# Performance work log

Measured on AMD Instinct MI355X. Metric: run time of the kernel, lower is better.

## Reference

```python
import jax, jax.numpy as jnp
import numpy as np

N_NODES = 10000
NEG_SLOPE = 0.2  # PyG GATv2Conv default


def gatv2(x, src, dst, Wl, bl, Wr, br, att, bias, n_nodes):
    """Single-head GATv2Conv (PyG defaults: heads=1, concat=True, self-loops added by caller)."""
    xl = x @ Wl + bl            # [N, dout] message source transform (lin_l)
    xr = x @ Wr + br            # [N, dout] target transform (lin_r)
    h = jax.nn.leaky_relu(xl[src] + xr[dst], NEG_SLOPE)   # [E, dout]
    e = h @ att                                            # [E] attention logits
    m = jax.ops.segment_max(e, dst, num_segments=n_nodes)  # per-target max
    ex = jnp.exp(e - m[dst])
    s = jax.ops.segment_sum(ex, dst, num_segments=n_nodes)
    alpha = ex / s[dst]                                    # segment softmax over incoming edges
    out = jax.ops.segment_sum(alpha[:, None] * xl[src], dst, num_segments=n_nodes)
    return out + bias


def _glorot(key, shape, scale=0.05):
    return jax.random.normal(key, shape, dtype=jnp.float32) * scale


def setup_inputs() -> dict:
    key = jax.random.key(0)
    ks = jax.random.split(key, 20)
    d_in, d0, d1 = 1000, 256, 128
    E = 320000
    x = jax.random.normal(ks[0], (N_NODES, d_in), dtype=jnp.float32)
    edge_index = jax.random.randint(ks[1], (2, E), 0, N_NODES, dtype=jnp.int64)
    return {
        "x": x,
        "edge_index": edge_index,
        # proj_in: d_in -> 256
        "Wpi": _glorot(ks[2], (d_in, d0)), "bpi": jnp.zeros((d0,), jnp.float32),
        # enc GATv2Conv 256 -> 128
        "Wl1": _glorot(ks[3], (d0, d1)), "bl1": jnp.zeros((d1,), jnp.float32),
        "Wr1": _glorot(ks[4], (d0, d1)), "br1": jnp.zeros((d1,), jnp.float32),
        "att1": _glorot(ks[5], (d1,)), "bias1": jnp.zeros((d1,), jnp.float32),
        # dec GATv2Conv 128 -> 256
        "Wl2": _glorot(ks[6], (d1, d0)), "bl2": jnp.zeros((d0,), jnp.float32),
        "Wr2": _glorot(ks[7], (d1, d0)), "br2": jnp.zeros((d0,), jnp.float32),
        "att2": _glorot(ks[8], (d0,)), "bias2": jnp.zeros((d0,), jnp.float32),
        # proj_out: 256 -> d_in
        "Wpo": _glorot(ks[9], (d0, d_in)), "bpo": jnp.zeros((d_in,), jnp.float32),
    }


def reference(x, edge_index, Wpi, bpi, Wl1, bl1, Wr1, br1, att1, bias1,
              Wl2, bl2, Wr2, br2, att2, bias2, Wpo, bpo):
    n = x.shape[0]
    # add self-loops (PyG GATv2Conv default add_self_loops=True)
    loops = jnp.arange(n, dtype=edge_index.dtype)
    src = jnp.concatenate([edge_index[0], loops])
    dst = jnp.concatenate([edge_index[1], loops])
    h = x @ Wpi + bpi
    z = gatv2(h, src, dst, Wl1, bl1, Wr1, br1, att1, bias1, n)
    d = gatv2(z, src, dst, Wl2, bl2, Wr2, br2, att2, bias2, n)
    x_hat = d @ Wpo + bpo
    return (x_hat, z)
```

## Files before the change

kernel.cpp:

```cpp
#include <hip/hip_runtime.h>
#include <math.h>

#define N_NODES 10000
#define MPAD    10112
#define D_IN    1000
#define KPAD_IN 1024
#define D0      256
#define D1      128
#define NPAD_OUT 1024
#define NEG_SLOPE 0.2f

typedef __attribute__((ext_vector_type(8))) short short8;
typedef __attribute__((ext_vector_type(4))) float f32x4;

__device__ __forceinline__ ushort f2bf(float f) {
  union { float f; unsigned u; } c; c.f = f;
  unsigned r = c.u + 0x7FFF + ((c.u >> 16) & 1);
  return (ushort)(r >> 16);
}
__device__ __forceinline__ float bf2f(ushort b) {
  union { unsigned u; float f; } c; c.u = ((unsigned)b) << 16;
  return c.f;
}


__global__ void count_kernel(const int* __restrict__ idx, int E, int n, int* __restrict__ counts) {
  int k = blockIdx.x * blockDim.x + threadIdx.x;
  int tot = E + n;
  if (k >= tot) return;
  int dst = (k < E) ? idx[E + k] : (k - E);
  atomicAdd(&counts[dst], 1);
}

__global__ void scan_kernel(const int* __restrict__ counts, int* __restrict__ offsets,
                            int* __restrict__ cursors, int n) {
  __shared__ int tsum[1024];
  int tid = threadIdx.x;
  int per = (n + 1023) / 1024;
  int start = tid * per;
  int end = start + per; if (end > n) end = n;
  int s = 0;
  for (int i = start; i < end; i++) s += counts[i];
  tsum[tid] = s;
  __syncthreads();
  for (int off = 1; off < 1024; off <<= 1) {
    int v = (tid >= off) ? tsum[tid - off] : 0;
    __syncthreads();
    if (tid >= off) tsum[tid] += v;
    __syncthreads();
  }
  int run = (tid == 0) ? 0 : tsum[tid - 1];
  for (int i = start; i < end; i++) {
    offsets[i] = run; cursors[i] = run;
    run += counts[i];
  }
  if (tid == 1023) offsets[n] = tsum[1023];
}

__global__ void scatter_kernel(const int* __restrict__ idx, int E, int n,
                               int* __restrict__ cursors, int* __restrict__ srcs) {
  int k = blockIdx.x * blockDim.x + threadIdx.x;
  int tot = E + n;
  if (k >= tot) return;
  int src, dst;
  if (k < E) { src = idx[k]; dst = idx[E + k]; }
  else       { src = k - E;  dst = src; }
  int pos = atomicAdd(&cursors[dst], 1);
  srcs[pos] = src;
}


#define T_WPI   (256 * 1024)
#define T_W1    (256 * 256)
#define T_W2    (512 * 128)
#define T_WPO   (1024 * 256)
#define OFF_W1  T_WPI
#define OFF_W2  (OFF_W1 + T_W1)
#define OFF_WPO (OFF_W2 + T_W2)
#define OFF_B   (OFF_WPO + T_WPO)
#define T_ALL   (OFF_B + 768)
#define CONV_T  (MPAD * 256)
#define PREP_T  (CONV_T + T_ALL + N_NODES)

__global__ void prep_all(const float* __restrict__ x, ushort* __restrict__ xb,
                         const float* __restrict__ Wpi,
                         const float* __restrict__ Wl1, const float* __restrict__ Wr1,
                         const float* __restrict__ Wl2, const float* __restrict__ Wr2,
                         const float* __restrict__ Wpo,
                         const float* __restrict__ bl1, const float* __restrict__ br1,
                         const float* __restrict__ bl2, const float* __restrict__ br2,
                         ushort* __restrict__ Wpi_t, ushort* __restrict__ W1cat,
                         ushort* __restrict__ W2cat, ushort* __restrict__ Wpo_t,
                         float* __restrict__ bcat1, float* __restrict__ bcat2,
                         int* __restrict__ counts) {
  int idx = blockIdx.x * 256 + threadIdx.x;
  if (idx < CONV_T) {
    int r = idx >> 8, k4 = (idx & 255) * 4;
    ushort4 o = {0, 0, 0, 0};
    if (r < N_NODES && k4 < D_IN) {
      float4 v = *(const float4*)(x + (size_t)r * D_IN + k4);
      o.x = f2bf(v.x); o.y = f2bf(v.y); o.z = f2bf(v.z); o.w = f2bf(v.w);
    }
    *(ushort4*)(xb + (size_t)idx * 4) = o;
    return;
  }
  int j = idx - CONV_T;
  if (j < OFF_W1) {
    int n = j >> 10, k = j & 1023;
    Wpi_t[j] = f2bf((k < 1000) ? Wpi[(size_t)k * 256 + n] : 0.f);
  } else if (j < OFF_W2) {
    int q = j - OFF_W1, n = q >> 8, k = q & 255;
    float v = (n < 128) ? Wl1[k * 128 + n] : Wr1[k * 128 + (n - 128)];
    W1cat[q] = f2bf(v);
  } else if (j < OFF_WPO) {
    int q = j - OFF_W2, n = q >> 7, k = q & 127;
    float v = (n < 256) ? Wl2[k * 256 + n] : Wr2[k * 256 + (n - 256)];
    W2cat[q] = f2bf(v);
  } else if (j < OFF_B) {
    int q = j - OFF_WPO, n = q >> 8, k = q & 255;
    Wpo_t[q] = f2bf((n < 1000) ? Wpo[(size_t)k * 1000 + n] : 0.f);
  } else if (j < T_ALL) {
    int q = j - OFF_B;
    if (q < 128)      bcat1[q] = bl1[q];
    else if (q < 256) bcat1[q] = br1[q - 128];
    else if (q < 512) bcat2[q - 256] = bl2[q - 256];
    else              bcat2[q - 256] = br2[q - 512];
  } else {
    int q = j - T_ALL;
    if (q < N_NODES) counts[q] = 0;
  }
}


template<int MODE>
__launch_bounds__(256)
__global__ void gemm_mfma(const ushort* __restrict__ A, int lda,
                          const ushort* __restrict__ Bt, int ldb,
                          const float* __restrict__ bias,
                          float* __restrict__ Cf, ushort* __restrict__ Cb, int ldp,
                          int M_valid, int N_valid, int K) {
  constexpr int BK = 32;
  __shared__ ushort As[64 * BK];
  __shared__ ushort Bs[64 * BK];
  const int tid  = threadIdx.x;
  const int lane = tid & 63, wave = tid >> 6;
  const int wr = wave >> 1, wc = wave & 1;
  const int bm = blockIdx.y * 64, bn = blockIdx.x * 64;
  const int r16 = lane & 15, kb = lane >> 4;

  f32x4 acc[2][2] = {};

  const int srow = tid >> 2;
  const int scol = (tid & 3) * 8;
  const ushort* Ag = A  + (size_t)(bm + srow) * lda + scol;
  const ushort* Bg = Bt + (size_t)(bn + srow) * ldb + scol;

  for (int k0 = 0; k0 < K; k0 += BK) {
    __builtin_amdgcn_global_load_lds((const __attribute__((address_space(1))) void*)(Ag + k0),
                                     (__attribute__((address_space(3))) void*)(As + tid * 8), 16, 0, 0);
    __builtin_amdgcn_global_load_lds((const __attribute__((address_space(1))) void*)(Bg + k0),
                                     (__attribute__((address_space(3))) void*)(Bs + tid * 8), 16, 0, 0);
    __syncthreads();

    short8 af[2], bfr[2];
    #pragma unroll
    for (int mi = 0; mi < 2; mi++)
      af[mi] = *(const short8*)(As + ((wr * 32 + mi * 16 + r16) * BK + kb * 8));
    #pragma unroll
    for (int ni = 0; ni < 2; ni++)
      bfr[ni] = *(const short8*)(Bs + ((wc * 32 + ni * 16 + r16) * BK + kb * 8));
    #pragma unroll
    for (int mi = 0; mi < 2; mi++)
      #pragma unroll
      for (int ni = 0; ni < 2; ni++)
        acc[mi][ni] = __builtin_amdgcn_mfma_f32_16x16x32_bf16(af[mi], bfr[ni], acc[mi][ni], 0, 0, 0);
    __syncthreads();
  }

  #pragma unroll
  for (int mi = 0; mi < 2; mi++) {
    const int row = bm + wr * 32 + mi * 16 + (lane >> 4) * 4;
    #pragma unroll
    for (int ni = 0; ni < 2; ni++) {
      const int col = bn + wc * 32 + ni * 16 + r16;
      const float bv = (col < N_valid) ? bias[col] : 0.f;
      #pragma unroll
      for (int r = 0; r < 4; r++) {
        const int gr = row + r;
        const float val = acc[mi][ni][r] + bv;
        if constexpr (MODE == 0) {
          if (gr < M_valid && col < N_valid) Cf[(size_t)gr * ldp + col] = val;
        } else if constexpr (MODE == 1) {
          Cb[(size_t)gr * ldp + col] = f2bf(gr < M_valid ? val : 0.f);
        } else {
          if (col < ldp) Cb[(size_t)gr * ldp + col] = f2bf(val);
          else           Cf[(size_t)gr * ldp + (col - ldp)] = val;
        }
      }
    }
  }
}


template<int D>
__launch_bounds__(256)
__global__ void gat_fused(const ushort* __restrict__ xlb, const float* __restrict__ xrf,
                          const float* __restrict__ att, const float* __restrict__ bias,
                          const int* __restrict__ offsets, const int* __restrict__ srcs,
                          float* __restrict__ out_f32, ushort* __restrict__ out_bf16,
                          int n_valid) {
  constexpr int EPL = D / 64;
  const int v    = blockIdx.x;
  const int tid  = threadIdx.x;
  const int lane = tid & 63;
  const int wave = tid >> 6;
  const int d0   = lane * EPL;

  if (v >= n_valid) {
    if (out_bf16 && tid < D) out_bf16[(size_t)v * D + tid] = 0;
    return;
  }

  __shared__ float m_s[4];
  __shared__ float s_s[4];
  __shared__ float buf[4][D];

  float rv[EPL], av[EPL], acc[EPL];
  #pragma unroll
  for (int d = 0; d < EPL; d++) {
    rv[d]  = xrf[(size_t)v * D + d0 + d];
    av[d]  = att[d0 + d];
    acc[d] = 0.f;
  }

  const int beg = offsets[v], end = offsets[v + 1];
  float m = -INFINITY, s = 0.f;

  int k = beg + wave;
  ushort xnxt[EPL];
  if (k < end) {
    const int u0 = srcs[k];
    if constexpr (EPL == 4) *(ushort4*)xnxt = *(const ushort4*)(xlb + (size_t)u0 * D + d0);
    else                    *(ushort2*)xnxt = *(const ushort2*)(xlb + (size_t)u0 * D + d0);
  }

  for (; k < end; k += 4) {
    ushort xcur[EPL];
    #pragma unroll
    for (int d = 0; d < EPL; d++) xcur[d] = xnxt[d];

    const int kn = k + 4;
    if (kn < end) {
      const int un = srcs[kn];
      if constexpr (EPL == 4) *(ushort4*)xnxt = *(const ushort4*)(xlb + (size_t)un * D + d0);
      else                    *(ushort2*)xnxt = *(const ushort2*)(xlb + (size_t)un * D + d0);
    }

    float xv[EPL], p = 0.f;
    #pragma unroll
    for (int d = 0; d < EPL; d++) {
      xv[d] = bf2f(xcur[d]);
      float t = xv[d] + rv[d];
      t = fmaxf(t, NEG_SLOPE * t);
      p = fmaf(t, av[d], p);
    }
    #pragma unroll
    for (int off = 32; off > 0; off >>= 1) p += __shfl_xor(p, off);

    if (p <= m + 8.f) {
      const float w = __expf(p - m);
      s += w;
      #pragma unroll
      for (int d = 0; d < EPL; d++) acc[d] = fmaf(w, xv[d], acc[d]);
    } else {
      const float cold = __expf(m - p);
      s = fmaf(s, cold, 1.f);
      #pragma unroll
      for (int d = 0; d < EPL; d++) acc[d] = fmaf(acc[d], cold, xv[d]);
      m = p;
    }
  }

  if (lane == 0) m_s[wave] = m;
  __syncthreads();
  const float M = fmaxf(fmaxf(m_s[0], m_s[1]), fmaxf(m_s[2], m_s[3]));
  const float c = __expf(m - M);
  if (lane == 0) s_s[wave] = s * c;
  #pragma unroll
  for (int d = 0; d < EPL; d++) buf[wave][d0 + d] = acc[d] * c;
  __syncthreads();

  if (tid < D) {
    const float stot = s_s[0] + s_s[1] + s_s[2] + s_s[3];
    const float val = (buf[0][tid] + buf[1][tid] + buf[2][tid] + buf[3][tid]) / stot + bias[tid];
    if (out_f32)  out_f32[(size_t)v * D + tid] = val;
    if (out_bf16) out_bf16[(size_t)v * D + tid] = f2bf(val);
  }
}


extern "C" void kernel_launch(void* const* d_in, const int* in_sizes, int n_in,
                              void* d_out, int out_size, void* d_ws, size_t ws_size,
                              hipStream_t stream) {
  const float* x     = (const float*)d_in[0];
  const int*   eidx  = (const int*)d_in[1];
  const float* Wpi   = (const float*)d_in[2];
  const float* bpi   = (const float*)d_in[3];
  const float* Wl1   = (const float*)d_in[4];
  const float* bl1   = (const float*)d_in[5];
  const float* Wr1   = (const float*)d_in[6];
  const float* br1   = (const float*)d_in[7];
  const float* att1  = (const float*)d_in[8];
  const float* bias1 = (const float*)d_in[9];
  const float* Wl2   = (const float*)d_in[10];
  const float* bl2   = (const float*)d_in[11];
  const float* Wr2   = (const float*)d_in[12];
  const float* br2   = (const float*)d_in[13];
  const float* att2  = (const float*)d_in[14];
  const float* bias2 = (const float*)d_in[15];
  const float* Wpo   = (const float*)d_in[16];
  const float* bpo   = (const float*)d_in[17];

  const int E    = in_sizes[1] / 2;
  const int n    = N_NODES;
  const int Etot = E + n;

  float* out_xhat = (float*)d_out;
  float* out_z    = (float*)d_out + (size_t)N_NODES * D_IN;

  char* wp = (char*)d_ws;
  auto alloc = [&](size_t bytes) { char* p = wp; wp += (bytes + 255) & ~(size_t)255; return p; };
  char* regionA = (char*)alloc((size_t)MPAD * KPAD_IN * 2);
  ushort* hb_db = (ushort*)alloc((size_t)MPAD * D0 * 2);
  ushort* zb    = (ushort*)alloc((size_t)MPAD * D1 * 2);
  int* counts  = (int*)alloc((size_t)n * 4);
  int* offsets = (int*)alloc((size_t)(n + 1) * 4);
  int* cursors = (int*)alloc((size_t)n * 4);
  int* srcs    = (int*)alloc((size_t)Etot * 4);
  ushort* Wpi_t = (ushort*)alloc((size_t)T_WPI * 2);
  ushort* W1cat = (ushort*)alloc((size_t)T_W1 * 2);
  ushort* W2cat = (ushort*)alloc((size_t)T_W2 * 2);
  ushort* Wpo_t = (ushort*)alloc((size_t)T_WPO * 2);
  float*  bcat1 = (float*)alloc(256 * 4);
  float*  bcat2 = (float*)alloc(512 * 4);

  ushort* xb   = (ushort*)regionA;
  float*  xr1f = (float*)regionA;
  ushort* xl1b = (ushort*)(regionA + 8 * 1024 * 1024);
  float*  xr2f = (float*)regionA;
  ushort* xl2b = (ushort*)(regionA + 12 * 1024 * 1024);
  ushort* hb   = hb_db;
  ushort* db   = hb_db;

  prep_all<<<(PREP_T + 255) / 256, 256, 0, stream>>>(
      x, xb, Wpi, Wl1, Wr1, Wl2, Wr2, Wpo, bl1, br1, bl2, br2,
      Wpi_t, W1cat, W2cat, Wpo_t, bcat1, bcat2, counts);
  const int tb = 256;
  count_kernel<<<(Etot + tb - 1) / tb, tb, 0, stream>>>(eidx, E, n, counts);
  scan_kernel<<<1, 1024, 0, stream>>>(counts, offsets, cursors, n);
  scatter_kernel<<<(Etot + tb - 1) / tb, tb, 0, stream>>>(eidx, E, n, cursors, srcs);

  gemm_mfma<1><<<dim3(D0 / 64, MPAD / 64), 256, 0, stream>>>(
      xb, KPAD_IN, Wpi_t, KPAD_IN, bpi, nullptr, hb, D0, N_NODES, D0, KPAD_IN);
  gemm_mfma<2><<<dim3(256 / 64, MPAD / 64), 256, 0, stream>>>(
      hb, D0, W1cat, D0, bcat1, xr1f, xl1b, D1, N_NODES, 256, D0);
  gat_fused<D1><<<MPAD, 256, 0, stream>>>(xl1b, xr1f, att1, bias1,
                                          offsets, srcs, out_z, zb, N_NODES);
  gemm_mfma<2><<<dim3(512 / 64, MPAD / 64), 256, 0, stream>>>(
      zb, D1, W2cat, D1, bcat2, xr2f, xl2b, D0, N_NODES, 512, D1);
  gat_fused<D0><<<MPAD, 256, 0, stream>>>(xl2b, xr2f, att2, bias2,
                                          offsets, srcs, nullptr, db, N_NODES);
  gemm_mfma<0><<<dim3(NPAD_OUT / 64, MPAD / 64), 256, 0, stream>>>(
      db, D0, Wpo_t, D0, bpo, out_xhat, nullptr, D_IN, N_NODES, D_IN, D0);
}
```

Before: 322.3 us.

## Process multiple edges per wave using sub-wave lane groups in GAT aggregation

Each wave in the fused GATv2 kernel is split into groups of D/16 lanes. Each lane handles 16 features through two 16-byte bf16 loads, so a block now processes 16 edges (D=256) or 32 edges (D=128) per step instead of 4. This cuts the shuffle reduction depth, widens memory accesses and raises edge-level parallelism. The data-dependent branch in the online softmax is replaced by branchless predicated updates. The cost is more registers and shared memory, a longer cross-group combine at the end, and wasted lanes at the tail for low-degree nodes.

Result: faster. 307.4 us (-4.6%).

```diff
diff --git a/kernel.cpp b/kernel.cpp
--- a/kernel.cpp
+++ b/kernel.cpp
@@ -209,90 +209,108 @@
                           const int* __restrict__ offsets, const int* __restrict__ srcs,
                           float* __restrict__ out_f32, ushort* __restrict__ out_bf16,
                           int n_valid) {
-  constexpr int EPL = D / 64;
+  constexpr int G    = D / 16;
+  constexpr int LOGG = (D == 256) ? 4 : 3;
+  constexpr int NGW  = 64 / G;
+  constexpr int NG   = 4 * NGW;
+  constexpr int H    = D / 2;
+
   const int v    = blockIdx.x;
   const int tid  = threadIdx.x;
   const int lane = tid & 63;
   const int wave = tid >> 6;
-  const int d0   = lane * EPL;
+  const int sub  = lane & (G - 1);
+  const int grp  = wave * NGW + (lane >> LOGG);
+  const int d0   = sub * 8;
 
   if (v >= n_valid) {
     if (out_bf16 && tid < D) out_bf16[(size_t)v * D + tid] = 0;
     return;
   }
 
-  __shared__ float m_s[4];
-  __shared__ float s_s[4];
-  __shared__ float buf[4][D];
-
-  float rv[EPL], av[EPL], acc[EPL];
+  __shared__ float m_s[NG];
+  __shared__ float s_s[NG];
+  __shared__ float buf[NG][D];
+
+  float rv[16], av[16], acc[16];
   #pragma unroll
-  for (int d = 0; d < EPL; d++) {
-    rv[d]  = xrf[(size_t)v * D + d0 + d];
-    av[d]  = att[d0 + d];
-    acc[d] = 0.f;
+  for (int i = 0; i < 8; i++) {
+    rv[i]     = xrf[(size_t)v * D + d0 + i];
+    rv[8 + i] = xrf[(size_t)v * D + H + d0 + i];
+    av[i]     = att[d0 + i];
+    av[8 + i] = att[H + d0 + i];
+    acc[i] = 0.f; acc[8 + i] = 0.f;
   }
 
   const int beg = offsets[v], end = offsets[v + 1];
-  float m = -INFINITY, s = 0.f;
-
-  int k = beg + wave;
-  ushort xnxt[EPL];
-  if (k < end) {
-    const int u0 = srcs[k];
-    if constexpr (EPL == 4) *(ushort4*)xnxt = *(const ushort4*)(xlb + (size_t)u0 * D + d0);
-    else                    *(ushort2*)xnxt = *(const ushort2*)(xlb + (size_t)u0 * D + d0);
-  }
-
-  for (; k < end; k += 4) {
-    ushort xcur[EPL];
-    #pragma unroll
-    for (int d = 0; d < EPL; d++) xcur[d] = xnxt[d];
-
-    const int kn = k + 4;
-    if (kn < end) {
-      const int un = srcs[kn];
-      if constexpr (EPL == 4) *(ushort4*)xnxt = *(const ushort4*)(xlb + (size_t)un * D + d0);
-      else                    *(ushort2*)xnxt = *(const ushort2*)(xlb + (size_t)un * D + d0);
+  float m = -1e30f, s = 0.f;
+
+  int k = beg + grp;
+  ushort xn[16];
+  {
+    const int ks = (k < end) ? k : beg;
+    const int u  = srcs[ks];
+    *(short8*)(xn)     = *(const short8*)(xlb + (size_t)u * D + d0);
+    *(short8*)(xn + 8) = *(const short8*)(xlb + (size_t)u * D + H + d0);
+  }
+
+  const int iters = (end - beg + NG - 1) / NG;
+  for (int it = 0; it < iters; it++, k += NG) {
+    const bool valid = (k < end);
+    ushort xc[16];
+    #pragma unroll
+    for (int i = 0; i < 16; i++) xc[i] = xn[i];
+
+    {
+      const int kn = k + NG;
+      const int ks = (kn < end) ? kn : beg;
+      const int u  = srcs[ks];
+      *(short8*)(xn)     = *(const short8*)(xlb + (size_t)u * D + d0);
+      *(short8*)(xn + 8) = *(const short8*)(xlb + (size_t)u * D + H + d0);
     }
 
-    float xv[EPL], p = 0.f;
-    #pragma unroll
-    for (int d = 0; d < EPL; d++) {
-      xv[d] = bf2f(xcur[d]);
-      float t = xv[d] + rv[d];
-      t = fmaxf(t, NEG_SLOPE * t);
-      p = fmaf(t, av[d], p);
+    float xv[16];
+    float p0 = 0.f, p1 = 0.f, p2 = 0.f, p3 = 0.f;
+    #pragma unroll
+    for (int i = 0; i < 4; i++) {
+      float t;
+      xv[i]      = bf2f(xc[i]);      t = xv[i]      + rv[i];      t = fmaxf(t, NEG_SLOPE * t); p0 = fmaf(t, av[i], p0);
+      xv[4 + i]  = bf2f(xc[4 + i]);  t = xv[4 + i]  + rv[4 + i];  t = fmaxf(t, NEG_SLOPE * t); p1 = fmaf(t, av[4 + i], p1);
+      xv[8 + i]  = bf2f(xc[8 + i]);  t = xv[8 + i]  + rv[8 + i];  t = fmaxf(t, NEG_SLOPE * t); p2 = fmaf(t, av[8 + i], p2);
+      xv[12 + i] = bf2f(xc[12 + i]); t = xv[12 + i] + rv[12 + i]; t = fmaxf(t, NEG_SLOPE * t); p3 = fmaf(t, av[12 + i], p3);
     }
-    #pragma unroll
-    for (int off = 32; off > 0; off >>= 1) p += __shfl_xor(p, off);
-
-    if (p <= m + 8.f) {
-      const float w = __expf(p - m);
-      s += w;
-      #pragma unroll
-      for (int d = 0; d < EPL; d++) acc[d] = fmaf(w, xv[d], acc[d]);
-    } else {
-      const float cold = __expf(m - p);
-      s = fmaf(s, cold, 1.f);
-      #pragma unroll
-      for (int d = 0; d < EPL; d++) acc[d] = fmaf(acc[d], cold, xv[d]);
-      m = p;
-    }
-  }
-
-  if (lane == 0) m_s[wave] = m;
+    float p = (p0 + p1) + (p2 + p3);
+    #pragma unroll
+    for (int off = G / 2; off > 0; off >>= 1) p += __shfl_xor(p, off);
+
+    const float m2   = valid ? fmaxf(m, p) : m;
+    const float cold = __expf(m - m2);
+    const float w    = valid ? __expf(p - m2) : 0.f;
+    s = fmaf(s, cold, w);
+    #pragma unroll
+    for (int d = 0; d < 16; d++) acc[d] = fmaf(acc[d], cold, w * xv[d]);
+    m = m2;
+  }
+
+  if (sub == 0) m_s[grp] = m;
   __syncthreads();
-  const float M = fmaxf(fmaxf(m_s[0], m_s[1]), fmaxf(m_s[2], m_s[3]));
+  float M = m_s[0];
+  #pragma unroll
+  for (int g = 1; g < NG; g++) M = fmaxf(M, m_s[g]);
   const float c = __expf(m - M);
-  if (lane == 0) s_s[wave] = s * c;
+  if (sub == 0) s_s[grp] = s * c;
   #pragma unroll
-  for (int d = 0; d < EPL; d++) buf[wave][d0 + d] = acc[d] * c;
+  for (int i = 0; i < 8; i++) {
+    buf[grp][d0 + i]     = acc[i] * c;
+    buf[grp][H + d0 + i] = acc[8 + i] * c;
+  }
   __syncthreads();
 
   if (tid < D) {
-    const float stot = s_s[0] + s_s[1] + s_s[2] + s_s[3];
-    const float val = (buf[0][tid] + buf[1][tid] + buf[2][tid] + buf[3][tid]) / stot + bias[tid];
+    float stot = 0.f, val = 0.f;
+    #pragma unroll
+    for (int g = 0; g < NG; g++) { stot += s_s[g]; val += buf[g][tid]; }
+    val = val / stot + bias[tid];
     if (out_f32)  out_f32[(size_t)v * D + tid] = val;
     if (out_bf16) out_bf16[(size_t)v * D + tid] = f2bf(val);
   }
```
